# Performance work log

Measured on AMD Instinct MI355X. Metric: run time of the kernel, lower is better.

Reference implementation:

```python
import jax, jax.numpy as jnp
import numpy as np

L, H, D, V, TMAX = 6, 16, 1024, 32000, 2048
HD = D // H
EPS = 1e-5


def _ln(x, g, b):
    m = jnp.mean(x, axis=-1, keepdims=True)
    v = jnp.var(x, axis=-1, keepdims=True)
    return (x - m) * jax.lax.rsqrt(v + EPS) * g + b


def setup_inputs() -> dict:
    key = jax.random.key(0)
    ks = jax.random.split(key, 16)
    s = 0.02
    inp = {
        'idx': jax.random.randint(ks[0], (2, TMAX), 0, V),
        'targets': jax.random.randint(ks[1], (2, TMAX), 0, V),
        'tok_emb': jax.random.normal(ks[2], (V, D), jnp.float32) * s,
        'pos_emb': jax.random.normal(ks[3], (TMAX, D), jnp.float32) * s,
        'wq': jax.random.normal(ks[4], (L, D, D), jnp.float32) * s,
        'wk': jax.random.normal(ks[5], (L, D, D), jnp.float32) * s,
        'wv': jax.random.normal(ks[6], (L, D, D), jnp.float32) * s,
        'w_proj': jax.random.normal(ks[7], (L, D, D), jnp.float32) * s,
        'b_proj': jnp.zeros((L, D), jnp.float32),
        'w_fc1': jax.random.normal(ks[8], (L, D, 4 * D), jnp.float32) * s,
        'b_fc1': jnp.zeros((L, 4 * D), jnp.float32),
        'w_fc2': jax.random.normal(ks[9], (L, 4 * D, D), jnp.float32) * s,
        'b_fc2': jnp.zeros((L, D), jnp.float32),
        'ln1_g': jnp.ones((L, D), jnp.float32), 'ln1_b': jnp.zeros((L, D), jnp.float32),
        'ln2_g': jnp.ones((L, D), jnp.float32), 'ln2_b': jnp.zeros((L, D), jnp.float32),
        'lnf_g': jnp.ones((D,), jnp.float32), 'lnf_b': jnp.zeros((D,), jnp.float32),
        'w_head': jax.random.normal(ks[10], (D, V), jnp.float32) * s,
        'b_head': jnp.zeros((V,), jnp.float32),
    }
    return inp


def reference(idx, targets, tok_emb, pos_emb, wq, wk, wv, w_proj, b_proj,
              w_fc1, b_fc1, w_fc2, b_fc2, ln1_g, ln1_b, ln2_g, ln2_b,
              lnf_g, lnf_b, w_head, b_head):
    B, T = idx.shape
    x = tok_emb[idx] + pos_emb[:T]  # [B,T,D]
    causal = jnp.tril(jnp.ones((T, T), bool))
    scale = HD ** -0.5
    for l in range(L):
        h = _ln(x, ln1_g[l], ln1_b[l])
        q = (h @ wq[l]).reshape(B, T, H, HD)
        k = (h @ wk[l]).reshape(B, T, H, HD)
        v = (h @ wv[l]).reshape(B, T, H, HD)
        att = jnp.einsum('bqhd,bkhd->bhqk', q, k) * scale
        att = jnp.where(causal, att, -jnp.inf)
        att = jax.nn.softmax(att, axis=-1)  # dropout is identity in eval
        o = jnp.einsum('bhqk,bkhd->bqhd', att, v).reshape(B, T, D)
        x = x + o @ w_proj[l] + b_proj[l]
        h = _ln(x, ln2_g[l], ln2_b[l])
        x = x + jax.nn.relu(h @ w_fc1[l] + b_fc1[l]) @ w_fc2[l] + b_fc2[l]
    x = _ln(x, lnf_g, lnf_b)
    logits = x @ w_head + b_head  # [B,T,V]
    logp = jax.nn.log_softmax(logits, axis=-1)
    nll = -jnp.take_along_axis(logp, targets[..., None], axis=-1)[..., 0]
    loss = jnp.mean(nll)
    return logits, loss
```

## Files before the change

kernel.cpp:

```cpp
#include <hip/hip_runtime.h>

#define LAYERS 6
#define NH 16
#define DIM 1024
#define VOCAB 32000
#define SEQ 2048
#define NBATCH 2
#define HEADD 64
#define NROW (NBATCH*SEQ)
#define FF 4096
#define QKVS 3072
#define NCB (VOCAB/256)
#define LN_EPS 1e-5f

typedef unsigned short bfu;
typedef __attribute__((ext_vector_type(8))) short s16x8;
typedef __attribute__((ext_vector_type(4))) float f32x4;

__device__ __forceinline__ float bf2f(bfu u) { return __uint_as_float(((unsigned)u) << 16); }
__device__ __forceinline__ bfu f2bf(float x) {
  unsigned u = __float_as_uint(x);
  return (bfu)((u + 0x7fffu + ((u >> 16) & 1u)) >> 16);
}

__device__ __forceinline__ void gload16(const void* g, void* l) {
  __builtin_amdgcn_global_load_lds((const __attribute__((address_space(1))) void*)g,
                                   (__attribute__((address_space(3))) void*)l, 16, 0, 0);
}

__device__ __forceinline__ f32x4 mfma32(s16x8 a, s16x8 b, f32x4 c) {
  return __builtin_amdgcn_mfma_f32_16x16x32_bf16(a, b, c, 0, 0, 0);
}

__global__ __launch_bounds__(256) void tkernel(const float* __restrict__ in,
                                               bfu* __restrict__ out, int R, int C) {
  __shared__ bfu tile[32][33];
  int tx = threadIdx.x, ty = threadIdx.y;
  int bx = blockIdx.x * 32, by = blockIdx.y * 32;
#pragma unroll
  for (int i = 0; i < 4; ++i)
    tile[ty + i * 8][tx] = f2bf(in[(size_t)(by + ty + i * 8) * C + bx + tx]);
  __syncthreads();
#pragma unroll
  for (int i = 0; i < 4; ++i)
    out[(size_t)(bx + ty + i * 8) * R + by + tx] = tile[tx][ty + i * 8];
}

__global__ __launch_bounds__(256) void wtrans_kernel(const float* __restrict__ wq,
                                                     const float* __restrict__ wk,
                                                     const float* __restrict__ wv,
                                                     const float* __restrict__ wp,
                                                     const float* __restrict__ w1,
                                                     const float* __restrict__ w2,
                                                     bfu* __restrict__ qkvT,
                                                     bfu* __restrict__ wpT,
                                                     bfu* __restrict__ f1T,
                                                     bfu* __restrict__ f2T) {
  __shared__ bfu tile[32][33];
  int bi = blockIdx.x;
  const float* in; bfu* out; int R, C, id;
  if (bi < 4096) {
    int p = bi >> 10; id = bi & 1023;
    in = p == 0 ? wq : p == 1 ? wk : p == 2 ? wv : wp;
    out = (p == 3) ? wpT : qkvT + (size_t)p * DIM * DIM;
    R = DIM; C = DIM;
  } else if (bi < 8192) {
    id = bi - 4096; in = w1; out = f1T; R = DIM; C = FF;
  } else {
    id = bi - 8192; in = w2; out = f2T; R = FF; C = DIM;
  }
  int nbx = C >> 5;
  int bx = (id % nbx) * 32, by = (id / nbx) * 32;
  int tx = threadIdx.x, ty = threadIdx.y;
#pragma unroll
  for (int i = 0; i < 4; ++i)
    tile[ty + i * 8][tx] = f2bf(in[(size_t)(by + ty + i * 8) * C + bx + tx]);
  __syncthreads();
#pragma unroll
  for (int i = 0; i < 4; ++i)
    out[(size_t)(bx + ty + i * 8) * R + by + tx] = tile[tx][ty + i * 8];
}

__global__ __launch_bounds__(256) void embed_kernel(const int* __restrict__ idx,
                                                    const float* __restrict__ tok,
                                                    const float* __restrict__ pos,
                                                    float* __restrict__ xf) {
  int row = blockIdx.x;
  int t = row % SEQ;
  int tokid = idx[row];
  int d0 = threadIdx.x * 4;
  float4 tv = *(const float4*)&tok[(size_t)tokid * DIM + d0];
  float4 pv = *(const float4*)&pos[(size_t)t * DIM + d0];
  float4 r;
  r.x = tv.x + pv.x; r.y = tv.y + pv.y; r.z = tv.z + pv.z; r.w = tv.w + pv.w;
  *(float4*)&xf[(size_t)row * DIM + d0] = r;
}

__global__ __launch_bounds__(256) void ln_kernel(const float* __restrict__ xf,
                                                 const float* __restrict__ gw,
                                                 const float* __restrict__ bw,
                                                 bfu* __restrict__ h) {
  const int row = blockIdx.x * 4 + (threadIdx.x >> 6);
  const int lane = threadIdx.x & 63;
  const float* xr = xf + (size_t)row * DIM;
  float4 xv[4];
  float s = 0.0f, ss = 0.0f;
#pragma unroll
  for (int j = 0; j < 4; ++j) {
    xv[j] = *(const float4*)&xr[lane * 4 + j * 256];
    s  += xv[j].x + xv[j].y + xv[j].z + xv[j].w;
    ss += xv[j].x * xv[j].x + xv[j].y * xv[j].y + xv[j].z * xv[j].z + xv[j].w * xv[j].w;
  }
#pragma unroll
  for (int o = 32; o; o >>= 1) { s += __shfl_xor(s, o); ss += __shfl_xor(ss, o); }
  float mean = s * (1.0f / DIM);
  float inv = rsqrtf(ss * (1.0f / DIM) - mean * mean + LN_EPS);
#pragma unroll
  for (int j = 0; j < 4; ++j) {
    float4 gv = *(const float4*)&gw[lane * 4 + j * 256];
    float4 bv = *(const float4*)&bw[lane * 4 + j * 256];
    ushort4 hv;
    hv.x = f2bf((xv[j].x - mean) * inv * gv.x + bv.x);
    hv.y = f2bf((xv[j].y - mean) * inv * gv.y + bv.y);
    hv.z = f2bf((xv[j].z - mean) * inv * gv.z + bv.z);
    hv.w = f2bf((xv[j].w - mean) * inv * gv.w + bv.w);
    *(ushort4*)&h[(size_t)row * DIM + lane * 4 + j * 256] = hv;
  }
}

__global__ __launch_bounds__(256) void lnfuse_kernel(float* __restrict__ xf,
                                                     const float* __restrict__ pb,
                                                     const float* __restrict__ bias,
                                                     const float* __restrict__ gw,
                                                     const float* __restrict__ bw,
                                                     bfu* __restrict__ h) {
  const int row = blockIdx.x * 4 + (threadIdx.x >> 6);
  const int lane = threadIdx.x & 63;
  float* xr = xf + (size_t)row * DIM;
  const float* p0 = pb + (size_t)row * DIM;
  const float* p1 = pb + (size_t)NROW * DIM + (size_t)row * DIM;
  float4 xv[4];
  float s = 0.0f, ss = 0.0f;
#pragma unroll
  for (int j = 0; j < 4; ++j) {
    int i0 = lane * 4 + j * 256;
    float4 a = *(const float4*)&xr[i0];
    float4 q0 = *(const float4*)&p0[i0];
    float4 q1 = *(const float4*)&p1[i0];
    float4 bb = *(const float4*)&bias[i0];
    xv[j].x = a.x + q0.x + q1.x + bb.x;
    xv[j].y = a.y + q0.y + q1.y + bb.y;
    xv[j].z = a.z + q0.z + q1.z + bb.z;
    xv[j].w = a.w + q0.w + q1.w + bb.w;
    *(float4*)&xr[i0] = xv[j];
    s  += xv[j].x + xv[j].y + xv[j].z + xv[j].w;
    ss += xv[j].x * xv[j].x + xv[j].y * xv[j].y + xv[j].z * xv[j].z + xv[j].w * xv[j].w;
  }
#pragma unroll
  for (int o = 32; o; o >>= 1) { s += __shfl_xor(s, o); ss += __shfl_xor(ss, o); }
  float mean = s * (1.0f / DIM);
  float inv = rsqrtf(ss * (1.0f / DIM) - mean * mean + LN_EPS);
#pragma unroll
  for (int j = 0; j < 4; ++j) {
    int i0 = lane * 4 + j * 256;
    float4 gv = *(const float4*)&gw[i0];
    float4 bv = *(const float4*)&bw[i0];
    ushort4 hv;
    hv.x = f2bf((xv[j].x - mean) * inv * gv.x + bv.x);
    hv.y = f2bf((xv[j].y - mean) * inv * gv.y + bv.y);
    hv.z = f2bf((xv[j].z - mean) * inv * gv.z + bv.z);
    hv.w = f2bf((xv[j].w - mean) * inv * gv.w + bv.w);
    *(ushort4*)&h[(size_t)row * DIM + i0] = hv;
  }
}

template <int MODE>
__global__ __launch_bounds__(256) void gemm_bt(const bfu* __restrict__ A,
                                               const bfu* __restrict__ Bt,
                                               const float* __restrict__ bias,
                                               const float* resid,
                                               void* outp,
                                               bfu* __restrict__ vT,
                                               int M, int N, int K, int ldk) {
  __shared__ __align__(16) char sm[32768];
  const int tid = threadIdx.x;
  const int lane = tid & 63, wave = tid >> 6;
  const int c = lane & 15, g = lane >> 4;

  const int gx = gridDim.x, gy = gridDim.y, gz = gridDim.z;
  int orig = (blockIdx.z * gy + blockIdx.y) * gx + blockIdx.x;
  int nwg = gx * gy * gz;
  int cpx = nwg >> 3;
  int swz = (orig & 7) * cpx + (orig >> 3);
  int bz = swz / (gx * gy);
  int rem = swz - bz * (gx * gy);
  int by = rem / gx, bx = rem - by * gx;

  const int m0 = by * 128, n0 = bx * 128;
  const int wm = (wave & 1) * 64, wn = (wave >> 1) * 64;
  f32x4 acc[4][4] = {};
  const char* Ac = (const char*)(A + (size_t)bz * K);
  const char* Bc = (const char*)(Bt + (size_t)bz * K);
  const size_t stride = (size_t)ldk * 2;

  const int g1 = tid, g2 = tid + 256;
  const int r1 = g1 >> 2, j1 = g1 & 3;
  const int r2 = g2 >> 2, j2 = g2 & 3;
  const size_t a1 = (size_t)(m0 + r1) * stride + j1 * 16;
  const size_t a2 = (size_t)(m0 + r2) * stride + j2 * 16;
  const size_t b1 = (size_t)(n0 + r1) * stride + j1 * 16;
  const size_t b2 = (size_t)(n0 + r2) * stride + j2 * 16;

  auto STAGE = [&](int kt, int buf) {
    char* base = sm + buf * 16384;
    size_t ko = (size_t)kt * 64;
    gload16(Ac + a1 + ko, base + g1 * 16);
    gload16(Ac + a2 + ko, base + g2 * 16);
    gload16(Bc + b1 + ko, base + 8192 + g1 * 16);
    gload16(Bc + b2 + ko, base + 8192 + g2 * 16);
  };

  const int NT = K >> 5;
  STAGE(0, 0);
  STAGE(1, 1);
  asm volatile("s_waitcnt vmcnt(4)" ::: "memory");
  __builtin_amdgcn_s_barrier();
  __builtin_amdgcn_sched_barrier(0);

  for (int i = 0; i < NT; ++i) {
    const char* base = sm + (i & 1) * 16384;
    s16x8 af[4], bfr[4];
#pragma unroll
    for (int mi = 0; mi < 4; ++mi)
      af[mi] = *(const s16x8*)(base + (wm + mi * 16 + c) * 64 + g * 16);
#pragma unroll
    for (int ni = 0; ni < 4; ++ni)
      bfr[ni] = *(const s16x8*)(base + 8192 + (wn + ni * 16 + c) * 64 + g * 16);
    asm volatile("s_waitcnt lgkmcnt(0)" ::: "memory");
    __builtin_amdgcn_sched_barrier(0);
    __builtin_amdgcn_s_barrier();
    __builtin_amdgcn_sched_barrier(0);
    if (i + 2 < NT) STAGE(i + 2, i & 1);
    __builtin_amdgcn_s_setprio(1);
#pragma unroll
    for (int mi = 0; mi < 4; ++mi)
#pragma unroll
      for (int ni = 0; ni < 4; ++ni)
        acc[mi][ni] = mfma32(af[mi], bfr[ni], acc[mi][ni]);
    __builtin_amdgcn_s_setprio(0);
    if (i < NT - 2) {
      asm volatile("s_waitcnt vmcnt(4)" ::: "memory");
      __builtin_amdgcn_s_barrier();
      __builtin_amdgcn_sched_barrier(0);
    } else if (i == NT - 2) {
      asm volatile("s_waitcnt vmcnt(0)" ::: "memory");
      __builtin_amdgcn_s_barrier();
      __builtin_amdgcn_sched_barrier(0);
    }
  }

#pragma unroll
  for (int mi = 0; mi < 4; ++mi) {
#pragma unroll
    for (int ni = 0; ni < 4; ++ni) {
      int col = n0 + wn + ni * 16 + c;
      float bv = (MODE != 6 && bias) ? bias[col] : 0.0f;
#pragma unroll
      for (int jj = 0; jj < 4; ++jj) {
        int row = m0 + wm + mi * 16 + g * 4 + jj;
        float val = acc[mi][ni][jj] + bv;
        size_t oi = (size_t)row * N + col;
        if (MODE == 1) val = fmaxf(val, 0.0f);
        if (MODE == 2)      ((float*)outp)[oi] = resid[oi] + val;
        else if (MODE == 6) ((float*)outp)[(size_t)bz * M * N + oi] = val;
        else {
          ((bfu*)outp)[oi] = f2bf(val);
          if (MODE == 5 && col >= 2048) {
            int d = col - 2048;
            int b2 = row >> 11, t = row & 2047;
            vT[((size_t)((b2 << 4) + (d >> 6)) * HEADD + (d & 63)) * SEQ + t] = f2bf(val);
          }
        }
      }
    }
  }
}

template <int MODE>
__global__ __launch_bounds__(1024) void gemm1024(const bfu* __restrict__ A,
                                                 const bfu* __restrict__ Bt,
                                                 const float* __restrict__ bias,
                                                 const float* resid,
                                                 void* outp,
                                                 int M, int N, int K,
                                                 int colchunk,
                                                 float* __restrict__ pmax,
                                                 float* __restrict__ psum) {
  extern __shared__ char smem[];
  const int tid = threadIdx.x;
  const int lane = tid & 63, w = tid >> 6;
  const int c = lane & 15, g = lane >> 4;

  const int gx = gridDim.x, gy = gridDim.y;
  int orig = blockIdx.y * gx + blockIdx.x;
  int cpx = (gx * gy) >> 3;
  int swz = (orig & 7) * cpx + (orig >> 3);
  int bx, by;
  if (colchunk) { bx = swz / gy; by = swz - bx * gy; }
  else          { by = swz / gx; bx = swz - by * gx; }
  const int m0 = by * 256, n0 = bx * 256;

  const int wrow = w >> 2, wcol = w & 3;
  const size_t gstr = (size_t)K * 2;
  const char* Ag = (const char*)A + (size_t)m0 * gstr;
  const char* Bg = (const char*)Bt + (size_t)n0 * gstr;

  int srow0 = tid >> 3, scg0 = (tid & 7) ^ (srow0 & 7);
  int srow1 = (tid + 1024) >> 3, scg1 = (tid & 7) ^ (srow1 & 7);
  const size_t ga0 = (size_t)srow0 * gstr + scg0 * 16;
  const size_t ga1 = (size_t)srow1 * gstr + scg1 * 16;

  auto STAGE = [&](int kt, int buf) {
    char* base = smem + buf * 65536;
    size_t ko = (size_t)kt * 128;
    gload16(Ag + ga0 + ko, base + w * 1024);
    gload16(Ag + ga1 + ko, base + 16384 + w * 1024);
    gload16(Bg + ga0 + ko, base + 32768 + w * 1024);
    gload16(Bg + ga1 + ko, base + 49152 + w * 1024);
  };

  const int NT = K >> 6;
  f32x4 acc[4][4] = {};

  STAGE(0, 0);
  STAGE(1, 1);
  asm volatile("s_waitcnt vmcnt(4)" ::: "memory");
  __builtin_amdgcn_s_barrier();
  __builtin_amdgcn_sched_barrier(0);

  const int rsw = (c & 7) << 4;
  const int off0 = (g * 16) ^ rsw;
  const int off1 = (64 + g * 16) ^ rsw;

  for (int i = 0; i < NT; ++i) {
    const char* ldsA = smem + (i & 1) * 65536 + (wrow * 64 + c) * 128;
    const char* ldsB = smem + (i & 1) * 65536 + 32768 + (wcol * 64 + c) * 128;
    s16x8 a[4], b[4];
#pragma unroll
    for (int mi = 0; mi < 4; ++mi) a[mi] = *(const s16x8*)(ldsA + mi * 2048 + off0);
#pragma unroll
    for (int ni = 0; ni < 4; ++ni) b[ni] = *(const s16x8*)(ldsB + ni * 2048 + off0);
    __builtin_amdgcn_s_setprio(1);
#pragma unroll
    for (int mi = 0; mi < 4; ++mi)
#pragma unroll
      for (int ni = 0; ni < 4; ++ni)
        acc[mi][ni] = mfma32(a[mi], b[ni], acc[mi][ni]);
    __builtin_amdgcn_s_setprio(0);
#pragma unroll
    for (int mi = 0; mi < 4; ++mi) a[mi] = *(const s16x8*)(ldsA + mi * 2048 + off1);
#pragma unroll
    for (int ni = 0; ni < 4; ++ni) b[ni] = *(const s16x8*)(ldsB + ni * 2048 + off1);
    asm volatile("s_waitcnt lgkmcnt(0)" ::: "memory");
    __builtin_amdgcn_sched_barrier(0);
    __builtin_amdgcn_s_barrier();
    __builtin_amdgcn_sched_barrier(0);
    if (i + 2 < NT) STAGE(i + 2, i & 1);
    __builtin_amdgcn_s_setprio(1);
#pragma unroll
    for (int mi = 0; mi < 4; ++mi)
#pragma unroll
      for (int ni = 0; ni < 4; ++ni)
        acc[mi][ni] = mfma32(a[mi], b[ni], acc[mi][ni]);
    __builtin_amdgcn_s_setprio(0);
    if (i < NT - 2) {
      asm volatile("s_waitcnt vmcnt(4)" ::: "memory");
      __builtin_amdgcn_s_barrier();
      __builtin_amdgcn_sched_barrier(0);
    } else if (i == NT - 2) {
      asm volatile("s_waitcnt vmcnt(0)" ::: "memory");
      __builtin_amdgcn_s_barrier();
      __builtin_amdgcn_sched_barrier(0);
    }
  }

  if (MODE != 4) {
#pragma unroll
    for (int mi = 0; mi < 4; ++mi) {
#pragma unroll
      for (int ni = 0; ni < 4; ++ni) {
        int col = n0 + wcol * 64 + ni * 16 + c;
        float bv = bias ? bias[col] : 0.0f;
#pragma unroll
        for (int jj = 0; jj < 4; ++jj) {
          int row = m0 + wrow * 64 + mi * 16 + g * 4 + jj;
          float val = acc[mi][ni][jj] + bv;
          size_t oi = (size_t)row * N + col;
          if (MODE == 1) val = fmaxf(val, 0.0f);
          else if (MODE == 2) { ((float*)outp)[oi] = resid[oi] + val; continue; }
          if (MODE == 3) ((float*)outp)[oi] = val;
          else           ((bfu*)outp)[oi] = f2bf(val);
        }
      }
    }
  } else {
    float* sred = (float*)(smem + 131072);
    const int ncb = N >> 8;
    float bvv[4]; int colv[4];
#pragma unroll
    for (int ni = 0; ni < 4; ++ni) {
      colv[ni] = n0 + wcol * 64 + ni * 16 + c;
      bvv[ni] = bias ? bias[colv[ni]] : 0.0f;
    }
#pragma unroll
    for (int mi = 0; mi < 4; ++mi) {
#pragma unroll
      for (int jj = 0; jj < 4; ++jj) {
        int row = m0 + wrow * 64 + mi * 16 + g * 4 + jj;
        float v[4];
#pragma unroll
        for (int ni = 0; ni < 4; ++ni) {
          v[ni] = acc[mi][ni][jj] + bvv[ni];
          ((float*)outp)[(size_t)row * N + colv[ni]] = v[ni];
        }
        float mx = fmaxf(fmaxf(v[0], v[1]), fmaxf(v[2], v[3]));
#pragma unroll
        for (int off = 1; off < 16; off <<= 1) mx = fmaxf(mx, __shfl_xor(mx, off));
        float sm = __expf(v[0] - mx) + __expf(v[1] - mx) +
                   __expf(v[2] - mx) + __expf(v[3] - mx);
#pragma unroll
        for (int off = 1; off < 16; off <<= 1) sm += __shfl_xor(sm, off);
        if (c == 0) {
          int r64 = mi * 16 + g * 4 + jj;
          sred[(w * 64 + r64) * 2 + 0] = mx;
          sred[(w * 64 + r64) * 2 + 1] = sm;
        }
      }
    }
    __syncthreads();
    if (tid < 256) {
      int wr = tid >> 6, r64 = tid & 63;
      float M2 = -3.0e38f, S2 = 0.0f;
#pragma unroll
      for (int wc2 = 0; wc2 < 4; ++wc2) {
        float m_i = sred[((wr * 4 + wc2) * 64 + r64) * 2 + 0];
        float s_i = sred[((wr * 4 + wc2) * 64 + r64) * 2 + 1];
        float nm = fmaxf(M2, m_i);
        S2 = S2 * __expf(M2 - nm) + s_i * __expf(m_i - nm);
        M2 = nm;
      }
      size_t pi = (size_t)(m0 + tid) * ncb + bx;
      pmax[pi] = M2;
      psum[pi] = S2;
    }
  }
}

__global__ __launch_bounds__(512) void attn_kernel(const bfu* __restrict__ qkv,
                                                   const bfu* __restrict__ vT,
                                                   bfu* __restrict__ o) {
  __shared__ __align__(16) bfu Ks[64 * 64];
  __shared__ __align__(16) bfu Vt[64 * 64];
  __shared__ __align__(16) bfu Plds[8 * 16 * 32];
  const int tid = threadIdx.x;
  const int lane = tid & 63, w = tid >> 6;
  const int c = lane & 15, g = lane >> 4;
  const int qt = blockIdx.x, hh = blockIdx.y, b = blockIdx.z;
  const int q0 = qt * 128 + w * 16;
  const float SENT = -1e30f;
  const size_t rowb = (size_t)b * SEQ;

  const size_t qbase = (rowb + q0 + c) * QKVS + hh * HEADD + g * 8;
  s16x8 qf0 = *(const s16x8*)&qkv[qbase];
  s16x8 qf1 = *(const s16x8*)&qkv[qbase + 32];
  const bfu* Kg = qkv + 1024 + hh * HEADD;
  const bfu* vTb = vT + (size_t)(b * NH + hh) * HEADD * SEQ;
  bfu* Pw = Plds + w * 512;

  const int srow = tid >> 3;
  const int sgr = (tid & 7) ^ (srow & 7);
  const int cw = c & 7;

  f32x4 oacc[4] = {};
  float mrun = SENT, lrun = 0.0f;

  const int nkt = 2 * qt + 2;
  for (int kt = 0; kt < nkt; ++kt) {
    const int k0 = kt * 64;
    __syncthreads();
    gload16(Kg + (rowb + k0 + srow) * QKVS + sgr * 8, (char*)Ks + w * 1024);
    gload16(vTb + (size_t)srow * SEQ + k0 + sgr * 8, (char*)Vt + w * 1024);
    asm volatile("s_waitcnt vmcnt(0)" ::: "memory");
    __syncthreads();

#pragma unroll
    for (int s = 0; s < 2; ++s) {
      const int k0s = k0 + s * 32;
      if (k0s <= q0 + 15) {
        const char* Kb = (const char*)Ks + (size_t)(s * 32 + c) * 128;
        s16x8 kf00 = *(const s16x8*)(Kb + ((g ^ cw) * 16));
        s16x8 kf01 = *(const s16x8*)(Kb + (((4 + g) ^ cw) * 16));
        s16x8 kf10 = *(const s16x8*)(Kb + 16 * 128 + ((g ^ cw) * 16));
        s16x8 kf11 = *(const s16x8*)(Kb + 16 * 128 + (((4 + g) ^ cw) * 16));
        f32x4 s0 = {}, s1 = {};
        s0 = mfma32(kf00, qf0, s0); s0 = mfma32(kf01, qf1, s0);
        s1 = mfma32(kf10, qf0, s1); s1 = mfma32(kf11, qf1, s1);

        float sv[8];
#pragma unroll
        for (int jj = 0; jj < 4; ++jj) {
          int ka = k0s + g * 4 + jj, kb = ka + 16;
          sv[jj]     = (ka <= q0 + c) ? s0[jj] * 0.125f : SENT;
          sv[4 + jj] = (kb <= q0 + c) ? s1[jj] * 0.125f : SENT;
        }
        float tmax = sv[0];
#pragma unroll
        for (int i = 1; i < 8; ++i) tmax = fmaxf(tmax, sv[i]);
        tmax = fmaxf(tmax, __shfl_xor(tmax, 16));
        tmax = fmaxf(tmax, __shfl_xor(tmax, 32));

        bool defer = __all(tmax <= mrun + 8.0f) && (kt | s);
        float mref = defer ? mrun : fmaxf(mrun, tmax);
        float p[8], psm = 0.0f;
#pragma unroll
        for (int i = 0; i < 8; ++i) { p[i] = __expf(sv[i] - mref); psm += p[i]; }
        psm += __shfl_xor(psm, 16);
        psm += __shfl_xor(psm, 32);

        ushort4 w0; w0.x = f2bf(p[0]); w0.y = f2bf(p[1]); w0.z = f2bf(p[2]); w0.w = f2bf(p[3]);
        ushort4 w1; w1.x = f2bf(p[4]); w1.y = f2bf(p[5]); w1.z = f2bf(p[6]); w1.w = f2bf(p[7]);
        *(ushort4*)&Pw[c * 32 + g * 4] = w0;
        *(ushort4*)&Pw[c * 32 + 16 + g * 4] = w1;
        asm volatile("s_waitcnt lgkmcnt(0)" ::: "memory");
        __builtin_amdgcn_sched_barrier(0);

        if (defer) {
          lrun += psm;
        } else {
          float mnew = mref;
          float alpha = __expf(mrun - mnew);
          lrun = lrun * alpha + psm;
          mrun = mnew;
          float aq[4];
#pragma unroll
          for (int jj = 0; jj < 4; ++jj) aq[jj] = __shfl(alpha, g * 4 + jj);
#pragma unroll
          for (int dg = 0; dg < 4; ++dg)
#pragma unroll
            for (int jj = 0; jj < 4; ++jj) oacc[dg][jj] *= aq[jj];
        }

        ushort4 ra = *(const ushort4*)&Pw[c * 32 + g * 8];
        ushort4 rb = *(const ushort4*)&Pw[c * 32 + g * 8 + 4];
        s16x8 pa = {(short)ra.x, (short)ra.y, (short)ra.z, (short)ra.w,
                    (short)rb.x, (short)rb.y, (short)rb.z, (short)rb.w};

#pragma unroll
        for (int dg = 0; dg < 4; ++dg) {
          s16x8 vf = *(const s16x8*)((const char*)Vt + (size_t)(dg * 16 + c) * 128 +
                                     (((s * 4 + g) ^ cw) * 16));
          oacc[dg] = mfma32(pa, vf, oacc[dg]);
        }
      }
    }
  }

  float lq[4];
#pragma unroll
  for (int jj = 0; jj < 4; ++jj) lq[jj] = __shfl(lrun, g * 4 + jj);
#pragma unroll
  for (int dg = 0; dg < 4; ++dg)
#pragma unroll
    for (int jj = 0; jj < 4; ++jj) {
      size_t oi = (size_t)(rowb + q0 + g * 4 + jj) * DIM + hh * HEADD + dg * 16 + c;
      o[oi] = f2bf(oacc[dg][jj] / lq[jj]);
    }
}

__global__ __launch_bounds__(64) void nll_finish(const float* __restrict__ pmax,
                                                 const float* __restrict__ psum,
                                                 const float* __restrict__ logits,
                                                 const int* __restrict__ tgt,
                                                 float* __restrict__ nll) {
  int row = blockIdx.x, lane = threadIdx.x;
  const float* pm = pmax + (size_t)row * NCB;
  const float* ps = psum + (size_t)row * NCB;
  float m = -3.0e38f, s = 0.0f;
  if (lane < NCB) { m = pm[lane]; s = ps[lane]; }
  int i2 = lane + 64;
  if (i2 < NCB) {
    float m2 = pm[i2], s2 = ps[i2];
    float nm = fmaxf(m, m2);
    s = s * __expf(m - nm) + s2 * __expf(m2 - nm);
    m = nm;
  }
#pragma unroll
  for (int off = 32; off; off >>= 1) {
    float om = __shfl_xor(m, off), os = __shfl_xor(s, off);
    float nm = fmaxf(m, om);
    s = s * __expf(m - nm) + os * __expf(om - nm);
    m = nm;
  }
  if (lane == 0)
    nll[row] = (m + __logf(s)) - logits[(size_t)row * VOCAB + tgt[row]];
}

__global__ __launch_bounds__(256) void loss_kernel(const float* __restrict__ nll,
                                                   float* __restrict__ out) {
  float s = 0.0f;
  for (int i = threadIdx.x; i < NROW; i += 256) s += nll[i];
  for (int off = 32; off; off >>= 1) s += __shfl_xor(s, off);
  __shared__ float r[4];
  int wave = threadIdx.x >> 6;
  if ((threadIdx.x & 63) == 0) r[wave] = s;
  __syncthreads();
  if (threadIdx.x == 0) out[(size_t)NROW * VOCAB] = (r[0] + r[1] + r[2] + r[3]) * (1.0f / NROW);
}

extern "C" void kernel_launch(void* const* d_in, const int* in_sizes, int n_in,
                              void* d_out, int out_size, void* d_ws, size_t ws_size,
                              hipStream_t stream) {
  (void)in_sizes; (void)n_in; (void)out_size;
  const int* idx       = (const int*)d_in[0];
  const int* targets   = (const int*)d_in[1];
  const float* tok_emb = (const float*)d_in[2];
  const float* pos_emb = (const float*)d_in[3];
  const float* wq      = (const float*)d_in[4];
  const float* wk      = (const float*)d_in[5];
  const float* wv      = (const float*)d_in[6];
  const float* w_proj  = (const float*)d_in[7];
  const float* b_proj  = (const float*)d_in[8];
  const float* w_fc1   = (const float*)d_in[9];
  const float* b_fc1   = (const float*)d_in[10];
  const float* w_fc2   = (const float*)d_in[11];
  const float* b_fc2   = (const float*)d_in[12];
  const float* ln1_g   = (const float*)d_in[13];
  const float* ln1_b   = (const float*)d_in[14];
  const float* ln2_g   = (const float*)d_in[15];
  const float* ln2_b   = (const float*)d_in[16];
  const float* lnf_g   = (const float*)d_in[17];
  const float* lnf_b   = (const float*)d_in[18];
  const float* w_head  = (const float*)d_in[19];
  const float* b_head  = (const float*)d_in[20];

  char* ws = (char*)d_ws;
  size_t off = 0;
  auto alloc = [&](size_t bytes) {
    char* p = ws + off;
    off += (bytes + 255) & ~(size_t)255;
    return p;
  };
  float* xf   = (float*)alloc((size_t)NROW * DIM * 4);
  bfu* hbuf   = (bfu*)alloc((size_t)NROW * DIM * 2);
  bfu* qkvb   = (bfu*)alloc((size_t)NROW * QKVS * 2);
  bfu* ob     = (bfu*)alloc((size_t)NROW * DIM * 2);
  bfu* ub     = (bfu*)alloc((size_t)NROW * FF * 2);
  bfu* vT     = (bfu*)alloc((size_t)NROW * DIM * 2);
  float* pbuf = (float*)alloc((size_t)2 * NROW * DIM * 4);
  bfu* qkvT   = (bfu*)alloc((size_t)QKVS * DIM * 2);
  bfu* wpT    = (bfu*)alloc((size_t)DIM * DIM * 2);
  bfu* f1T    = (bfu*)alloc((size_t)DIM * FF * 2);
  bfu* f2T    = (bfu*)alloc((size_t)DIM * FF * 2);
  bfu* hT     = (bfu*)alloc((size_t)DIM * VOCAB * 2);
  float* nll  = (float*)alloc((size_t)NROW * 4);
  float* pmax = (float*)alloc((size_t)NROW * NCB * 4);
  float* psum = (float*)alloc((size_t)NROW * NCB * 4);
  if (off > ws_size) return;

  const size_t LDSB = 131072;
  dim3 tb(32, 8);
  tkernel<<<dim3(VOCAB / 32, DIM / 32), tb, 0, stream>>>(w_head, hT, DIM, VOCAB);
  embed_kernel<<<NROW, 256, 0, stream>>>(idx, tok_emb, pos_emb, xf);

  float* logits = (float*)d_out;
  for (int l = 0; l < LAYERS; ++l) {
    const size_t wo = (size_t)l * DIM * DIM, fo = (size_t)l * DIM * FF;
    wtrans_kernel<<<12288, tb, 0, stream>>>(wq + wo, wk + wo, wv + wo, w_proj + wo,
                                            w_fc1 + fo, w_fc2 + fo, qkvT, wpT, f1T, f2T);
    if (l == 0)
      ln_kernel<<<NROW / 4, 256, 0, stream>>>(xf, ln1_g, ln1_b, hbuf);
    else
      lnfuse_kernel<<<NROW / 4, 256, 0, stream>>>(xf, pbuf, b_fc2 + (l - 1) * DIM,
                                                  ln1_g + l * DIM, ln1_b + l * DIM, hbuf);
    gemm_bt<5><<<dim3(QKVS / 128, NROW / 128), 256, 0, stream>>>(
        hbuf, qkvT, nullptr, nullptr, qkvb, vT, NROW, QKVS, DIM, DIM);
    attn_kernel<<<dim3(SEQ / 128, NH, NBATCH), 512, 0, stream>>>(qkvb, vT, ob);
    gemm_bt<6><<<dim3(DIM / 128, NROW / 128, 2), 256, 0, stream>>>(
        ob, wpT, nullptr, nullptr, pbuf, nullptr, NROW, DIM, DIM / 2, DIM);
    lnfuse_kernel<<<NROW / 4, 256, 0, stream>>>(xf, pbuf, b_proj + l * DIM,
                                                ln2_g + l * DIM, ln2_b + l * DIM, hbuf);
    gemm1024<1><<<dim3(FF / 256, NROW / 256), 1024, LDSB, stream>>>(
        hbuf, f1T, b_fc1 + l * FF, nullptr, ub, NROW, FF, DIM, 0, nullptr, nullptr);
    gemm_bt<6><<<dim3(DIM / 128, NROW / 128, 2), 256, 0, stream>>>(
        ub, f2T, nullptr, nullptr, pbuf, nullptr, NROW, DIM, FF / 2, FF);
  }

  lnfuse_kernel<<<NROW / 4, 256, 0, stream>>>(xf, pbuf, b_fc2 + 5 * DIM, lnf_g, lnf_b, hbuf);
  gemm1024<4><<<dim3(VOCAB / 256, NROW / 256), 1024, LDSB + 8192, stream>>>(
      hbuf, hT, b_head, nullptr, logits, NROW, VOCAB, DIM, 1, pmax, psum);
  nll_finish<<<NROW, 64, 0, stream>>>(pmax, psum, logits, targets, nll);
  loss_kernel<<<1, 256, 0, stream>>>(nll, logits);
}
```

Measured before the change: 1.961 ms.

## Add 8-wave 256x256 LM-head GEMM with larger per-wave tiles and fused softmax partials

Replaces the 1024-thread gemm1024 MODE 4 path for the vocabulary projection with a new 512-thread kernel. Each wave now computes a 128x64 tile (8x4 MFMA accumulators), and K-slab loads are double-buffered with XOR-swizzled LDS layout and explicit vmcnt waits. The per-row max/sum partials for the log-softmax are reduced in the epilogue as before. More accumulators per wave raise register pressure and may lower occupancy, in exchange for more MFMA work per LDS read.

```diff
diff --git a/kernel.cpp b/kernel.cpp
--- a/kernel.cpp
+++ b/kernel.cpp
@@ -384,75 +384,193 @@
     }
   }
 
-  if (MODE != 4) {
-#pragma unroll
-    for (int mi = 0; mi < 4; ++mi) {
-#pragma unroll
-      for (int ni = 0; ni < 4; ++ni) {
-        int col = n0 + wcol * 64 + ni * 16 + c;
-        float bv = bias ? bias[col] : 0.0f;
-#pragma unroll
-        for (int jj = 0; jj < 4; ++jj) {
-          int row = m0 + wrow * 64 + mi * 16 + g * 4 + jj;
-          float val = acc[mi][ni][jj] + bv;
-          size_t oi = (size_t)row * N + col;
-          if (MODE == 1) val = fmaxf(val, 0.0f);
-          else if (MODE == 2) { ((float*)outp)[oi] = resid[oi] + val; continue; }
-          if (MODE == 3) ((float*)outp)[oi] = val;
-          else           ((bfu*)outp)[oi] = f2bf(val);
-        }
-      }
-    }
-  } else {
-    float* sred = (float*)(smem + 131072);
-    const int ncb = N >> 8;
-    float bvv[4]; int colv[4];
+#pragma unroll
+  for (int mi = 0; mi < 4; ++mi) {
 #pragma unroll
     for (int ni = 0; ni < 4; ++ni) {
-      colv[ni] = n0 + wcol * 64 + ni * 16 + c;
-      bvv[ni] = bias ? bias[colv[ni]] : 0.0f;
-    }
-#pragma unroll
-    for (int mi = 0; mi < 4; ++mi) {
+      int col = n0 + wcol * 64 + ni * 16 + c;
+      float bv = bias ? bias[col] : 0.0f;
 #pragma unroll
       for (int jj = 0; jj < 4; ++jj) {
         int row = m0 + wrow * 64 + mi * 16 + g * 4 + jj;
-        float v[4];
-#pragma unroll
-        for (int ni = 0; ni < 4; ++ni) {
-          v[ni] = acc[mi][ni][jj] + bvv[ni];
-          ((float*)outp)[(size_t)row * N + colv[ni]] = v[ni];
-        }
-        float mx = fmaxf(fmaxf(v[0], v[1]), fmaxf(v[2], v[3]));
-#pragma unroll
-        for (int off = 1; off < 16; off <<= 1) mx = fmaxf(mx, __shfl_xor(mx, off));
-        float sm = __expf(v[0] - mx) + __expf(v[1] - mx) +
-                   __expf(v[2] - mx) + __expf(v[3] - mx);
-#pragma unroll
-        for (int off = 1; off < 16; off <<= 1) sm += __shfl_xor(sm, off);
-        if (c == 0) {
-          int r64 = mi * 16 + g * 4 + jj;
-          sred[(w * 64 + r64) * 2 + 0] = mx;
-          sred[(w * 64 + r64) * 2 + 1] = sm;
-        }
+        float val = acc[mi][ni][jj] + bv;
+        size_t oi = (size_t)row * N + col;
+        if (MODE == 1) val = fmaxf(val, 0.0f);
+        else if (MODE == 2) { ((float*)outp)[oi] = resid[oi] + val; continue; }
+        if (MODE == 3) ((float*)outp)[oi] = val;
+        else if (MODE != 1) ((bfu*)outp)[oi] = f2bf(val);
+        else ((bfu*)outp)[oi] = f2bf(val);
       }
     }
-    __syncthreads();
-    if (tid < 256) {
-      int wr = tid >> 6, r64 = tid & 63;
-      float M2 = -3.0e38f, S2 = 0.0f;
-#pragma unroll
-      for (int wc2 = 0; wc2 < 4; ++wc2) {
-        float m_i = sred[((wr * 4 + wc2) * 64 + r64) * 2 + 0];
-        float s_i = sred[((wr * 4 + wc2) * 64 + r64) * 2 + 1];
-        float nm = fmaxf(M2, m_i);
-        S2 = S2 * __expf(M2 - nm) + s_i * __expf(m_i - nm);
-        M2 = nm;
+  }
+}
+
+__global__ __launch_bounds__(512) void gemm8p(const bfu* __restrict__ A,
+                                              const bfu* __restrict__ Bt,
+                                              const float* __restrict__ bias,
+                                              float* __restrict__ outp,
+                                              int M, int N, int K,
+                                              float* __restrict__ pmax,
+                                              float* __restrict__ psum) {
+  extern __shared__ char smem[];
+  const int tid = threadIdx.x;
+  const int lane = tid & 63, w = tid >> 6;
+  const int c = lane & 15, g = lane >> 4;
+
+  const int gx = gridDim.x, gy = gridDim.y;
+  int orig = blockIdx.y * gx + blockIdx.x;
+  int cpx = (gx * gy) >> 3;
+  int swz = (orig & 7) * cpx + (orig >> 3);
+  int bx = swz / gy, by = swz - bx * gy;
+  const int m0 = by * 256, n0 = bx * 256;
+  const int wrow = w >> 2, wcol = w & 3;
+
+  const size_t gstr = (size_t)K * 2;
+  const char* Ag = (const char*)A + (size_t)m0 * gstr;
+  const char* Bg = (const char*)Bt + (size_t)n0 * gstr;
+
+  const int r0 = tid >> 2, j0 = tid & 3;
+  const int r1 = (tid + 512) >> 2;
+  const int f0 = (r0 ^ (r0 >> 2)) & 3, f1 = (r1 ^ (r1 >> 2)) & 3;
+  const size_t ga0 = (size_t)r0 * gstr + (size_t)(j0 ^ f0) * 16;
+  const size_t ga1 = (size_t)r1 * gstr + (size_t)(j0 ^ f1) * 16;
+
+  auto STAGE = [&](int t, int s) {
+    char* base = smem + (t & 1) * 65536;
+    char* As = base + s * 16384;
+    char* Bs = base + 32768 + s * 16384;
+    size_t ko = (size_t)t * 128 + (size_t)s * 64;
+    gload16(Ag + ga0 + ko, As + tid * 16);
+    gload16(Ag + ga1 + ko, As + (tid + 512) * 16);
+    gload16(Bg + ga0 + ko, Bs + tid * 16);
+    gload16(Bg + ga1 + ko, Bs + (tid + 512) * 16);
+  };
+
+  int aoff[8], boff[4];
+#pragma unroll
+  for (int mi = 0; mi < 8; ++mi) {
+    int ra = wrow * 128 + mi * 16 + c;
+    aoff[mi] = ra * 64 + ((g ^ ((ra ^ (ra >> 2)) & 3)) << 4);
+  }
+#pragma unroll
+  for (int ni = 0; ni < 4; ++ni) {
+    int rb = wcol * 64 + ni * 16 + c;
+    boff[ni] = rb * 64 + ((g ^ ((rb ^ (rb >> 2)) & 3)) << 4);
+  }
+
+  const int NT = K >> 6;
+  f32x4 acc[8][4] = {};
+
+  STAGE(0, 0); STAGE(0, 1); STAGE(1, 0);
+
+#define PHASE8(SLAB, BUFBASE)                                              \
+  {                                                                        \
+    const char* As_ = (BUFBASE) + (SLAB) * 16384;                          \
+    const char* Bs_ = (BUFBASE) + 32768 + (SLAB) * 16384;                  \
+    s16x8 a_[8], b_[4];                                                    \
+    _Pragma("unroll")                                                      \
+    for (int mi = 0; mi < 8; ++mi) a_[mi] = *(const s16x8*)(As_ + aoff[mi]); \
+    _Pragma("unroll")                                                      \
+    for (int ni = 0; ni < 4; ++ni) b_[ni] = *(const s16x8*)(Bs_ + boff[ni]); \
+    if (st_t >= 0) STAGE(st_t, st_s);                                      \
+    __builtin_amdgcn_s_setprio(1);                                         \
+    _Pragma("unroll")                                                      \
+    for (int mi = 0; mi < 8; ++mi)                                         \
+      _Pragma("unroll")                                                    \
+      for (int ni = 0; ni < 4; ++ni)                                       \
+        acc[mi][ni] = mfma32(a_[mi], b_[ni], acc[mi][ni]);                 \
+    __builtin_amdgcn_s_setprio(0);                                         \
+  }
+
+  for (int kt = 0; kt < NT - 1; ++kt) {
+    char* bufbase = smem + (kt & 1) * 65536;
+    asm volatile("s_waitcnt vmcnt(8)" ::: "memory");
+    __builtin_amdgcn_sched_barrier(0);
+    __builtin_amdgcn_s_barrier();
+    __builtin_amdgcn_sched_barrier(0);
+    {
+      int st_t = kt + 1, st_s = 1;
+      PHASE8(0, bufbase)
+    }
+    asm volatile("s_waitcnt vmcnt(8)" ::: "memory");
+    __builtin_amdgcn_sched_barrier(0);
+    __builtin_amdgcn_s_barrier();
+    __builtin_amdgcn_sched_barrier(0);
+    {
+      int st_t = (kt + 2 < NT) ? kt + 2 : -1, st_s = 0;
+      PHASE8(1, bufbase)
+    }
+  }
+  {
+    char* bufbase = smem + ((NT - 1) & 1) * 65536;
+    asm volatile("s_waitcnt vmcnt(4)" ::: "memory");
+    __builtin_amdgcn_sched_barrier(0);
+    __builtin_amdgcn_s_barrier();
+    __builtin_amdgcn_sched_barrier(0);
+    {
+      int st_t = -1, st_s = 0;
+      PHASE8(0, bufbase)
+    }
+    asm volatile("s_waitcnt vmcnt(0)" ::: "memory");
+    __builtin_amdgcn_sched_barrier(0);
+    __builtin_amdgcn_s_barrier();
+    __builtin_amdgcn_sched_barrier(0);
+    {
+      int st_t = -1, st_s = 0;
+      PHASE8(1, bufbase)
+    }
+  }
+#undef PHASE8
+
+  float* sred = (float*)(smem + 131072);
+  const int ncb = N >> 8;
+  float bvv[4]; int colv[4];
+#pragma unroll
+  for (int ni = 0; ni < 4; ++ni) {
+    colv[ni] = n0 + wcol * 64 + ni * 16 + c;
+    bvv[ni] = bias ? bias[colv[ni]] : 0.0f;
+  }
+#pragma unroll
+  for (int mi = 0; mi < 8; ++mi) {
+#pragma unroll
+    for (int jj = 0; jj < 4; ++jj) {
+      int r128 = mi * 16 + g * 4 + jj;
+      int row = m0 + wrow * 128 + r128;
+      float v[4];
+#pragma unroll
+      for (int ni = 0; ni < 4; ++ni) {
+        v[ni] = acc[mi][ni][jj] + bvv[ni];
+        outp[(size_t)row * N + colv[ni]] = v[ni];
       }
-      size_t pi = (size_t)(m0 + tid) * ncb + bx;
-      pmax[pi] = M2;
-      psum[pi] = S2;
-    }
+      float mx = fmaxf(fmaxf(v[0], v[1]), fmaxf(v[2], v[3]));
+#pragma unroll
+      for (int off = 1; off < 16; off <<= 1) mx = fmaxf(mx, __shfl_xor(mx, off));
+      float sm = __expf(v[0] - mx) + __expf(v[1] - mx) +
+                 __expf(v[2] - mx) + __expf(v[3] - mx);
+#pragma unroll
+      for (int off = 1; off < 16; off <<= 1) sm += __shfl_xor(sm, off);
+      if (c == 0) {
+        sred[(w * 128 + r128) * 2 + 0] = mx;
+        sred[(w * 128 + r128) * 2 + 1] = sm;
+      }
+    }
+  }
+  __syncthreads();
+  if (tid < 256) {
+    int wrow_r = tid >> 7, r128 = tid & 127;
+    float M2 = -3.0e38f, S2 = 0.0f;
+#pragma unroll
+    for (int wc2 = 0; wc2 < 4; ++wc2) {
+      int wi = wrow_r * 4 + wc2;
+      float m_i = sred[(wi * 128 + r128) * 2 + 0];
+      float s_i = sred[(wi * 128 + r128) * 2 + 1];
+      float nm = fmaxf(M2, m_i);
+      S2 = S2 * __expf(M2 - nm) + s_i * __expf(m_i - nm);
+      M2 = nm;
+    }
+    size_t pi = (size_t)(m0 + tid) * ncb + bx;
+    pmax[pi] = M2;
+    psum[pi] = S2;
   }
 }
 
@@ -696,8 +814,8 @@
   }
 
   lnfuse_kernel<<<NROW / 4, 256, 0, stream>>>(xf, pbuf, b_fc2 + 5 * DIM, lnf_g, lnf_b, hbuf);
-  gemm1024<4><<<dim3(VOCAB / 256, NROW / 256), 1024, LDSB + 8192, stream>>>(
-      hbuf, hT, b_head, nullptr, logits, NROW, VOCAB, DIM, 1, pmax, psum);
+  gemm8p<<<dim3(VOCAB / 256, NROW / 256), 512, 139264, stream>>>(
+      hbuf, hT, b_head, logits, NROW, VOCAB, DIM, pmax, psum);
   nll_finish<<<NROW, 64, 0, stream>>>(pmax, psum, logits, targets, nll);
   loss_kernel<<<1, 256, 0, stream>>>(nll, logits);
 }
```

Measured after the change: 1.994 ms. Within noise of the previous version (+1.7%).
